# Performance work log

Measured on AMD Instinct MI355X. Metric: run time of the kernel, lower is better.

Reference implementation:

```python
import jax, jax.numpy as jnp
import numpy as np

N_NODES = 100000


def setup_inputs() -> dict:
    key = jax.random.key(0)
    k1, k2, k3, k4, k5, k6 = jax.random.split(key, 6)
    x = jax.random.normal(k1, (N_NODES, 256), dtype=jnp.float32)
    edge_index = jax.random.randint(k2, (2, 3200000), 0, N_NODES, dtype=jnp.int64)
    # GCNConv(256, 3): glorot weight + zero bias (PyG default)
    lim1 = float(np.sqrt(6.0 / (256 + 3)))
    W1 = jax.random.uniform(k3, (256, 3), minval=-lim1, maxval=lim1, dtype=jnp.float32)
    b1 = jnp.zeros((3,), dtype=jnp.float32)
    # Linear(3, 7): torch default kaiming-uniform-ish bounds
    lim2 = float(1.0 / np.sqrt(3))
    W2 = jax.random.uniform(k4, (3, 7), minval=-lim2, maxval=lim2, dtype=jnp.float32)
    b2 = jax.random.uniform(k5, (7,), minval=-lim2, maxval=lim2, dtype=jnp.float32)
    return {"x": x, "edge_index": edge_index, "W1": W1, "b1": b1, "W2": W2, "b2": b2}


def gcn_conv(x, edge_index, W, b, num_nodes):
    # PyG GCNConv: add self-loops, symmetric deg^-1/2 (A+I) deg^-1/2 normalization,
    # aggregate transformed features, then add bias.
    loop = jnp.arange(num_nodes, dtype=edge_index.dtype)
    src = jnp.concatenate([edge_index[0], loop])
    dst = jnp.concatenate([edge_index[1], loop])
    ones = jnp.ones_like(dst, dtype=x.dtype)
    deg = jax.ops.segment_sum(ones, dst, num_segments=num_nodes)  # [N]
    dinv = jnp.where(deg > 0, jax.lax.rsqrt(deg), 0.0)
    norm = dinv[src] * dinv[dst]  # [E+N]
    h = x @ W  # [N, 3] — transform BEFORE gather (small width)
    msg = h[src] * norm[:, None]  # [E+N, 3]
    agg = jax.ops.segment_sum(msg, dst, num_segments=num_nodes)  # [N, 3]
    return agg + b


def reference(x, edge_index, W1, b1, W2, b2):
    h = jax.nn.relu(gcn_conv(x, edge_index, W1, b1, x.shape[0]))  # [N, 3]
    z = h @ W2 + b2  # [N, 7]
    return (h, z)
```

## Files before the change

kernel.cpp:

```cpp
#include <hip/hip_runtime.h>
#include <stdint.h>


#define BSHIFT 8
#define BNODES 256
#define OVFCAP 32768

__device__ __forceinline__ bool ei_is64(const unsigned* __restrict__ ei) {
    const int t = threadIdx.x;
    const int nz = (t < 256) && (ei[2 * t + 1] != 0u);
    return __syncthreads_or(nz) == 0;
}

__global__ __launch_bounds__(512) void k_pre(const float* __restrict__ x,
                                             const float* __restrict__ W1,
                                             float* __restrict__ g4,
                                             const unsigned* __restrict__ ei,
                                             unsigned* __restrict__ gcount,
                                             unsigned* __restrict__ records,
                                             unsigned* __restrict__ ovf,
                                             int E, int B, int CAP, int CH,
                                             int nbin, int N) {
    const bool is64 = ei_is64(ei);
    if ((int)blockIdx.x < nbin) {
        __shared__ unsigned cnt[512], base[512], cursor[512];
        const int e0 = blockIdx.x * CH;
        const int e1 = min(E, e0 + CH);
        for (int i = threadIdx.x; i < B; i += 512) { cnt[i] = 0u; cursor[i] = 0u; }
        __syncthreads();
        const unsigned long long* e64 = (const unsigned long long*)ei;
        for (int e = e0 + threadIdx.x; e < e1; e += 512) {
            const unsigned d = is64 ? (unsigned)e64[(size_t)E + e] : ei[(size_t)E + e];
            atomicAdd(&cnt[d >> BSHIFT], 1u);
        }
        __syncthreads();
        for (int i = threadIdx.x; i < B; i += 512)
            base[i] = cnt[i] ? atomicAdd(&gcount[i], cnt[i]) : 0u;
        __syncthreads();
        unsigned* ovf_cnt = gcount + B;
        for (int e = e0 + threadIdx.x; e < e1; e += 512) {
            unsigned s, d;
            if (is64) { s = (unsigned)e64[e]; d = (unsigned)e64[(size_t)E + e]; }
            else      { s = ei[e];            d = ei[(size_t)E + e]; }
            const unsigned bb  = d >> BSHIFT;
            const unsigned idx = base[bb] + atomicAdd(&cursor[bb], 1u);
            if (idx < (unsigned)CAP) {
                records[(size_t)bb * CAP + idx] = (s << BSHIFT) | (d & (BNODES - 1));
            } else {
                const unsigned o = atomicAdd(ovf_cnt, 1u);
                if (o < (unsigned)OVFCAP) { ovf[2 * o] = s; ovf[2 * o + 1] = d; }
            }
        }
    } else {
        const int bx      = blockIdx.x - nbin;
        const int gtid    = bx * 512 + threadIdx.x;
        const int nthread = ((int)gridDim.x - nbin) * 512;
        const int lane    = threadIdx.x & 63;
        float w[4][3];
#pragma unroll
        for (int k = 0; k < 4; ++k)
#pragma unroll
            for (int c = 0; c < 3; ++c)
                w[k][c] = W1[(lane * 4 + k) * 3 + c];
        const int wave   = gtid >> 6;
        const int nwaves = nthread >> 6;
        for (int node = wave; node < N; node += nwaves) {
            const float4 v = *reinterpret_cast<const float4*>(x + (size_t)node * 256 + lane * 4);
            float s0 = v.x * w[0][0] + v.y * w[1][0] + v.z * w[2][0] + v.w * w[3][0];
            float s1 = v.x * w[0][1] + v.y * w[1][1] + v.z * w[2][1] + v.w * w[3][1];
            float s2 = v.x * w[0][2] + v.y * w[1][2] + v.z * w[2][2] + v.w * w[3][2];
#pragma unroll
            for (int off = 32; off > 0; off >>= 1) {
                s0 += __shfl_xor(s0, off, 64);
                s1 += __shfl_xor(s1, off, 64);
                s2 += __shfl_xor(s2, off, 64);
            }
            if (lane == 0)
                reinterpret_cast<float4*>(g4)[node] = make_float4(s0, s1, s2, 0.f);
        }
    }
}

__global__ __launch_bounds__(256) void k_cnt2(const unsigned* __restrict__ gcount,
                                              const unsigned* __restrict__ records,
                                              const unsigned* __restrict__ ovf,
                                              unsigned* __restrict__ pcount,
                                              int B, int CAP, int SPLIT) {
    __shared__ unsigned cnt[BNODES];
    const int b  = blockIdx.x / SPLIT;
    const int sl = blockIdx.x - b * SPLIT;
    cnt[threadIdx.x] = 0u;
    __syncthreads();
    unsigned n = gcount[b]; if (n > (unsigned)CAP) n = CAP;
    const unsigned chunk = (n + SPLIT - 1) / SPLIT;
    const unsigned lo = sl * chunk;
    const unsigned hi = (lo + chunk < n) ? lo + chunk : n;
    const unsigned* rec = records + (size_t)b * CAP;
    for (unsigned i = lo + threadIdx.x; i < hi; i += 256)
        atomicAdd(&cnt[rec[i] & (BNODES - 1)], 1u);
    if (sl == 0) {
        unsigned no = gcount[B]; if (no > (unsigned)OVFCAP) no = OVFCAP;
        for (unsigned i = threadIdx.x; i < no; i += 256) {
            const unsigned d = ovf[2 * i + 1];
            if ((int)(d >> BSHIFT) == b) atomicAdd(&cnt[d & (BNODES - 1)], 1u);
        }
    }
    __syncthreads();
    pcount[((size_t)blockIdx.x << BSHIFT) + threadIdx.x] = cnt[threadIdx.x];
}

__global__ __launch_bounds__(256) void k_dinv2(const unsigned* __restrict__ pcount,
                                               float* __restrict__ g4, int N, int SPLIT) {
    const int i = blockIdx.x * 256 + threadIdx.x;
    if (i >= N) return;
    const int b = i >> BSHIFT, t = i & (BNODES - 1);
    unsigned deg = 1u;
    for (int s = 0; s < SPLIT; ++s)
        deg += pcount[(((size_t)b * SPLIT + s) << BSHIFT) + t];
    const float r = rsqrtf((float)deg);
    const float4 h = reinterpret_cast<const float4*>(g4)[i];
    reinterpret_cast<float4*>(g4)[i] = make_float4(h.x * r, h.y * r, h.z * r, r);
}

__global__ __launch_bounds__(256) void k_msg2(const unsigned* __restrict__ gcount,
                                              const unsigned* __restrict__ records,
                                              const unsigned* __restrict__ ovf,
                                              const float* __restrict__ g4,
                                              float* __restrict__ psum,
                                              int B, int CAP, int SPLIT) {
    __shared__ float acc[BNODES * 3];
    const int b  = blockIdx.x / SPLIT;
    const int sl = blockIdx.x - b * SPLIT;
    for (int i = threadIdx.x; i < BNODES * 3; i += 256) acc[i] = 0.f;
    __syncthreads();
    unsigned n = gcount[b]; if (n > (unsigned)CAP) n = CAP;
    const unsigned chunk = (n + SPLIT - 1) / SPLIT;
    const unsigned lo = sl * chunk;
    const unsigned hi = (lo + chunk < n) ? lo + chunk : n;
    const unsigned* rec = records + (size_t)b * CAP;
    const float4* g4v = reinterpret_cast<const float4*>(g4);
    unsigned i = lo + threadIdx.x;
    for (; i + 256 < hi; i += 512) {
        const unsigned r0 = rec[i], r1 = rec[i + 256];
        const float4 ga = g4v[r0 >> BSHIFT];
        const float4 gb = g4v[r1 >> BSHIFT];
        const unsigned l0 = (r0 & (BNODES - 1)) * 3, l1 = (r1 & (BNODES - 1)) * 3;
        atomicAdd(&acc[l0 + 0], ga.x); atomicAdd(&acc[l0 + 1], ga.y); atomicAdd(&acc[l0 + 2], ga.z);
        atomicAdd(&acc[l1 + 0], gb.x); atomicAdd(&acc[l1 + 1], gb.y); atomicAdd(&acc[l1 + 2], gb.z);
    }
    if (i < hi) {
        const unsigned r0 = rec[i];
        const float4 ga = g4v[r0 >> BSHIFT];
        const unsigned l0 = (r0 & (BNODES - 1)) * 3;
        atomicAdd(&acc[l0 + 0], ga.x); atomicAdd(&acc[l0 + 1], ga.y); atomicAdd(&acc[l0 + 2], ga.z);
    }
    if (sl == 0) {
        unsigned no = gcount[B]; if (no > (unsigned)OVFCAP) no = OVFCAP;
        for (unsigned k = threadIdx.x; k < no; k += 256) {
            const unsigned d = ovf[2 * k + 1];
            if ((int)(d >> BSHIFT) == b) {
                const float4 g = g4v[ovf[2 * k]];
                const unsigned l = (d & (BNODES - 1)) * 3;
                atomicAdd(&acc[l + 0], g.x); atomicAdd(&acc[l + 1], g.y); atomicAdd(&acc[l + 2], g.z);
            }
        }
    }
    __syncthreads();
    const size_t base = ((size_t)blockIdx.x * 3) << BSHIFT;
    psum[base +   0 + threadIdx.x] = acc[threadIdx.x * 3 + 0];
    psum[base + 256 + threadIdx.x] = acc[threadIdx.x * 3 + 1];
    psum[base + 512 + threadIdx.x] = acc[threadIdx.x * 3 + 2];
}

__global__ __launch_bounds__(256) void k_fin(const float* __restrict__ psum,
                                             const float* __restrict__ g4,
                                             const float* __restrict__ b1,
                                             const float* __restrict__ W2,
                                             const float* __restrict__ b2,
                                             float* __restrict__ out, int N, int SPLIT) {
    const int i = blockIdx.x * 256 + threadIdx.x;
    if (i >= N) return;
    const int b = i >> BSHIFT, t = i & (BNODES - 1);
    float a0 = 0.f, a1 = 0.f, a2 = 0.f;
    for (int s = 0; s < SPLIT; ++s) {
        const size_t base = (((size_t)b * SPLIT + s) * 3) << BSHIFT;
        a0 += psum[base + t];
        a1 += psum[base + 256 + t];
        a2 += psum[base + 512 + t];
    }
    const float4 g = reinterpret_cast<const float4*>(g4)[i];
    const float  r = g.w;
    const float h0 = fmaxf(r * (a0 + g.x) + b1[0], 0.f);
    const float h1 = fmaxf(r * (a1 + g.y) + b1[1], 0.f);
    const float h2 = fmaxf(r * (a2 + g.z) + b1[2], 0.f);
    out[3 * (size_t)i + 0] = h0;
    out[3 * (size_t)i + 1] = h1;
    out[3 * (size_t)i + 2] = h2;
    float* z = out + (size_t)3 * N;
#pragma unroll
    for (int c = 0; c < 7; ++c)
        z[7 * (size_t)i + c] = h0 * W2[c] + h1 * W2[7 + c] + h2 * W2[14 + c] + b2[c];
}

__global__ __launch_bounds__(256) void k_xw1_fb(const float* __restrict__ x,
                                                const float* __restrict__ W1,
                                                float* __restrict__ g4,
                                                unsigned* __restrict__ zptr,
                                                int nzero, int N) {
    const int gtid = blockIdx.x * 256 + threadIdx.x;
    const int nthread = gridDim.x * 256;
    for (int i = gtid; i < nzero; i += nthread) zptr[i] = 0u;
    const int lane = threadIdx.x & 63;
    float w[4][3];
#pragma unroll
    for (int k = 0; k < 4; ++k)
#pragma unroll
        for (int c = 0; c < 3; ++c) w[k][c] = W1[(lane * 4 + k) * 3 + c];
    const int wave = gtid >> 6, nwaves = nthread >> 6;
    for (int node = wave; node < N; node += nwaves) {
        const float4 v = *reinterpret_cast<const float4*>(x + (size_t)node * 256 + lane * 4);
        float s0 = v.x * w[0][0] + v.y * w[1][0] + v.z * w[2][0] + v.w * w[3][0];
        float s1 = v.x * w[0][1] + v.y * w[1][1] + v.z * w[2][1] + v.w * w[3][1];
        float s2 = v.x * w[0][2] + v.y * w[1][2] + v.z * w[2][2] + v.w * w[3][2];
#pragma unroll
        for (int off = 32; off > 0; off >>= 1) {
            s0 += __shfl_xor(s0, off, 64);
            s1 += __shfl_xor(s1, off, 64);
            s2 += __shfl_xor(s2, off, 64);
        }
        if (lane == 0)
            reinterpret_cast<float4*>(g4)[node] = make_float4(s0, s1, s2, 0.f);
    }
}
__global__ __launch_bounds__(256) void k_deg_fb(const unsigned* __restrict__ ei,
                                                float* __restrict__ deg, int E) {
    const bool is64 = ei_is64(ei);
    const int e = blockIdx.x * 256 + threadIdx.x;
    if (e >= E) return;
    const unsigned d = is64 ? (unsigned)((const unsigned long long*)ei)[(size_t)E + e]
                            : ei[(size_t)E + e];
    atomicAdd(&deg[d], 1.0f);
}
__global__ __launch_bounds__(256) void k_dinv_fb(const float* __restrict__ deg,
                                                 float* __restrict__ g4, int N) {
    const int i = blockIdx.x * 256 + threadIdx.x;
    if (i >= N) return;
    const float r = rsqrtf(1.0f + deg[i]);
    const float4 h = reinterpret_cast<const float4*>(g4)[i];
    reinterpret_cast<float4*>(g4)[i] = make_float4(h.x * r, h.y * r, h.z * r, r);
}
__global__ __launch_bounds__(256) void k_edge_fb(const unsigned* __restrict__ ei,
                                                 const float* __restrict__ g4,
                                                 float* __restrict__ u4, int E) {
    const bool is64 = ei_is64(ei);
    const int e = blockIdx.x * 256 + threadIdx.x;
    if (e >= E) return;
    unsigned s, d;
    if (is64) {
        const unsigned long long* q = (const unsigned long long*)ei;
        s = (unsigned)q[e]; d = (unsigned)q[(size_t)E + e];
    } else {
        s = ei[e]; d = ei[(size_t)E + e];
    }
    const float4 g = reinterpret_cast<const float4*>(g4)[s];
    atomicAdd(&u4[4 * (size_t)d + 0], g.x);
    atomicAdd(&u4[4 * (size_t)d + 1], g.y);
    atomicAdd(&u4[4 * (size_t)d + 2], g.z);
}
__global__ __launch_bounds__(256) void k_final_fb(const float* __restrict__ u4,
                                                  const float* __restrict__ g4,
                                                  const float* __restrict__ b1,
                                                  const float* __restrict__ W2,
                                                  const float* __restrict__ b2,
                                                  float* __restrict__ out, int N) {
    const int i = blockIdx.x * 256 + threadIdx.x;
    if (i >= N) return;
    const float4 g = reinterpret_cast<const float4*>(g4)[i];
    const float4 u = reinterpret_cast<const float4*>(u4)[i];
    const float  r = g.w;
    const float h0 = fmaxf(r * (u.x + g.x) + b1[0], 0.f);
    const float h1 = fmaxf(r * (u.y + g.y) + b1[1], 0.f);
    const float h2 = fmaxf(r * (u.z + g.z) + b1[2], 0.f);
    out[3 * (size_t)i + 0] = h0;
    out[3 * (size_t)i + 1] = h1;
    out[3 * (size_t)i + 2] = h2;
    float* z = out + (size_t)3 * N;
#pragma unroll
    for (int c = 0; c < 7; ++c)
        z[7 * (size_t)i + c] = h0 * W2[c] + h1 * W2[7 + c] + h2 * W2[14 + c] + b2[c];
}

extern "C" void kernel_launch(void* const* d_in, const int* in_sizes, int n_in,
                              void* d_out, int out_size, void* d_ws, size_t ws_size,
                              hipStream_t stream) {
    const float*    x   = (const float*)d_in[0];
    const unsigned* ei  = (const unsigned*)d_in[1];
    const float*    W1  = (const float*)d_in[2];
    const float*    b1  = (const float*)d_in[3];
    const float*    W2  = (const float*)d_in[4];
    const float*    b2  = (const float*)d_in[5];
    float*          out = (float*)d_out;

    const int N = in_sizes[0] / 256;
    const int E = in_sizes[1] / 2;
    const int B = (N + BNODES - 1) >> BSHIFT;

    char*     ws     = (char*)d_ws;
    unsigned* gcount = (unsigned*)ws;
    size_t off = (4ull * (B + 1) + 255) & ~(size_t)255;
    float*    g4  = (float*)(ws + off);
    off = (off + 16ull * N + 255) & ~(size_t)255;
    unsigned* ovf = (unsigned*)(ws + off);
    off = (off + 8ull * OVFCAP + 255) & ~(size_t)255;
    const size_t puoff = off;

    int SPLIT = 0, CAP = 0;
    size_t rec_off = 0;
    const int sps[4] = {8, 4, 2, 1};
    for (int si = 0; si < 4; ++si) {
        const int sp = sps[si];
        const size_t ro = (puoff + 4ull * B * sp * 768 + 255) & ~(size_t)255;
        if (ws_size < ro + 4096) continue;
        long cap = (long)((ws_size - ro) / (4ull * B));
        if (cap > 12288) cap = 12288;
        if (cap >= 8960) { SPLIT = sp; CAP = (int)cap; rec_off = ro; break; }
    }

    if (SPLIT) {
        unsigned* pcount  = (unsigned*)(ws + puoff);
        float*    psum    = (float*)(ws + puoff);
        unsigned* records = (unsigned*)(ws + rec_off);
        hipMemsetAsync(gcount, 0, 4ull * (B + 1), stream);
        const int CH   = 16384;
        const int nbin = (E + CH - 1) / CH;
        const int NBX  = 2048;
        k_pre<<<nbin + NBX, 512, 0, stream>>>(x, W1, g4, ei, gcount, records, ovf,
                                              E, B, CAP, CH, nbin, N);
        k_cnt2<<<B * SPLIT, 256, 0, stream>>>(gcount, records, ovf, pcount, B, CAP, SPLIT);
        k_dinv2<<<(N + 255) / 256, 256, 0, stream>>>(pcount, g4, N, SPLIT);
        k_msg2<<<B * SPLIT, 256, 0, stream>>>(gcount, records, ovf, g4, psum, B, CAP, SPLIT);
        k_fin<<<(N + 255) / 256, 256, 0, stream>>>(psum, g4, b1, W2, b2, out, N, SPLIT);
    } else {
        float* deg = (float*)(ws + puoff);
        float* u4  = deg + N;
        k_xw1_fb<<<4096, 256, 0, stream>>>(x, W1, g4, (unsigned*)deg, 5 * N, N);
        k_deg_fb<<<(E + 255) / 256, 256, 0, stream>>>(ei, deg, E);
        k_dinv_fb<<<(N + 255) / 256, 256, 0, stream>>>(deg, g4, N);
        k_edge_fb<<<(E + 255) / 256, 256, 0, stream>>>(ei, g4, u4, E);
        k_final_fb<<<(N + 255) / 256, 256, 0, stream>>>(u4, g4, b1, W2, b2, out, N);
    }
}
```

Measured before the change: 118.4 us.

## Replace global-atomic bucket binning with fixed per-block slots in a single pass

The edge binning in k_pre no longer does a count pass followed by a global atomicAdd per bucket to reserve ranges. Each of about 190 edge chunks now writes straight into a fixed 64-slot region per destination bucket, and records its per-bucket fill count in a pcnt table. Edges are read once, using vectorized uint4 or ulonglong2 loads. The count and message kernels scan the full fixed-capacity bucket layout and skip empty slots using the pcnt counts. This removes the second pass over the edge list and the global atomics, at the cost of scanning padded slots. Any bucket that exceeds its 64 slots goes to a smaller overflow list, which is scanned serially.

```diff
diff --git a/kernel.cpp b/kernel.cpp
--- a/kernel.cpp
+++ b/kernel.cpp
@@ -4,7 +4,9 @@
 
 #define BSHIFT 8
 #define BNODES 256
-#define OVFCAP 32768
+#define OVFCAP 8192
+#define STRIDE 64
+#define PSTRIDE 192
 
 __device__ __forceinline__ bool ei_is64(const unsigned* __restrict__ ei) {
     const int t = threadIdx.x;
@@ -16,41 +18,63 @@
                                              const float* __restrict__ W1,
                                              float* __restrict__ g4,
                                              const unsigned* __restrict__ ei,
-                                             unsigned* __restrict__ gcount,
                                              unsigned* __restrict__ records,
+                                             unsigned* __restrict__ pcnt,
+                                             unsigned* __restrict__ ovf_cnt,
                                              unsigned* __restrict__ ovf,
                                              int E, int B, int CAP, int CH,
                                              int nbin, int N) {
     const bool is64 = ei_is64(ei);
     if ((int)blockIdx.x < nbin) {
-        __shared__ unsigned cnt[512], base[512], cursor[512];
+        __shared__ unsigned cursor[512];
+        for (int i = threadIdx.x; i < B; i += 512) cursor[i] = 0u;
+        __syncthreads();
         const int e0 = blockIdx.x * CH;
         const int e1 = min(E, e0 + CH);
-        for (int i = threadIdx.x; i < B; i += 512) { cnt[i] = 0u; cursor[i] = 0u; }
-        __syncthreads();
-        const unsigned long long* e64 = (const unsigned long long*)ei;
-        for (int e = e0 + threadIdx.x; e < e1; e += 512) {
-            const unsigned d = is64 ? (unsigned)e64[(size_t)E + e] : ei[(size_t)E + e];
-            atomicAdd(&cnt[d >> BSHIFT], 1u);
+        const unsigned sbase = blockIdx.x * STRIDE;
+
+        auto emit = [&](unsigned s, unsigned d) {
+            const unsigned bb  = d >> BSHIFT;
+            const unsigned idx = atomicAdd(&cursor[bb], 1u);
+            if (idx < STRIDE) {
+                records[(size_t)bb * CAP + sbase + idx] = (s << BSHIFT) | (d & (BNODES - 1));
+            } else {
+                const unsigned o = atomicAdd(ovf_cnt, 1u);
+                if (o < OVFCAP) { ovf[2 * o] = s; ovf[2 * o + 1] = d; }
+            }
+        };
+
+        const int nq = (e1 - e0) >> 2;
+        if (is64) {
+            const unsigned long long* e64 = (const unsigned long long*)ei;
+            const ulonglong2* sp = (const ulonglong2*)(e64 + e0);
+            const ulonglong2* dp = (const ulonglong2*)(e64 + (size_t)E + e0);
+            for (int q = threadIdx.x; q < nq; q += 512) {
+                const ulonglong2 sa = sp[2 * q], sb = sp[2 * q + 1];
+                const ulonglong2 da = dp[2 * q], db = dp[2 * q + 1];
+                emit((unsigned)sa.x, (unsigned)da.x);
+                emit((unsigned)sa.y, (unsigned)da.y);
+                emit((unsigned)sb.x, (unsigned)db.x);
+                emit((unsigned)sb.y, (unsigned)db.y);
+            }
+            for (int e = e0 + 4 * nq + threadIdx.x; e < e1; e += 512)
+                emit((unsigned)e64[e], (unsigned)e64[(size_t)E + e]);
+        } else {
+            const uint4* sp = (const uint4*)(ei + e0);
+            const uint4* dp = (const uint4*)(ei + (size_t)E + e0);
+            for (int q = threadIdx.x; q < nq; q += 512) {
+                const uint4 s4 = sp[q], d4 = dp[q];
+                emit(s4.x, d4.x);
+                emit(s4.y, d4.y);
+                emit(s4.z, d4.z);
+                emit(s4.w, d4.w);
+            }
+            for (int e = e0 + 4 * nq + threadIdx.x; e < e1; e += 512)
+                emit(ei[e], ei[(size_t)E + e]);
         }
         __syncthreads();
         for (int i = threadIdx.x; i < B; i += 512)
-            base[i] = cnt[i] ? atomicAdd(&gcount[i], cnt[i]) : 0u;
-        __syncthreads();
-        unsigned* ovf_cnt = gcount + B;
-        for (int e = e0 + threadIdx.x; e < e1; e += 512) {
-            unsigned s, d;
-            if (is64) { s = (unsigned)e64[e]; d = (unsigned)e64[(size_t)E + e]; }
-            else      { s = ei[e];            d = ei[(size_t)E + e]; }
-            const unsigned bb  = d >> BSHIFT;
-            const unsigned idx = base[bb] + atomicAdd(&cursor[bb], 1u);
-            if (idx < (unsigned)CAP) {
-                records[(size_t)bb * CAP + idx] = (s << BSHIFT) | (d & (BNODES - 1));
-            } else {
-                const unsigned o = atomicAdd(ovf_cnt, 1u);
-                if (o < (unsigned)OVFCAP) { ovf[2 * o] = s; ovf[2 * o + 1] = d; }
-            }
-        }
+            pcnt[(size_t)i * PSTRIDE + blockIdx.x] = min(cursor[i], (unsigned)STRIDE);
     } else {
         const int bx      = blockIdx.x - nbin;
         const int gtid    = bx * 512 + threadIdx.x;
@@ -81,25 +105,28 @@
     }
 }
 
-__global__ __launch_bounds__(256) void k_cnt2(const unsigned* __restrict__ gcount,
-                                              const unsigned* __restrict__ records,
+__global__ __launch_bounds__(256) void k_cnt2(const unsigned* __restrict__ records,
+                                              const unsigned* __restrict__ pcnt,
+                                              const unsigned* __restrict__ ovf_cnt,
                                               const unsigned* __restrict__ ovf,
                                               unsigned* __restrict__ pcount,
-                                              int B, int CAP, int SPLIT) {
+                                              int B, int CAP, int SPLIT, int nbin) {
     __shared__ unsigned cnt[BNODES];
+    __shared__ unsigned scnt[PSTRIDE];
     const int b  = blockIdx.x / SPLIT;
     const int sl = blockIdx.x - b * SPLIT;
     cnt[threadIdx.x] = 0u;
+    for (int i = threadIdx.x; i < nbin; i += 256) scnt[i] = pcnt[(size_t)b * PSTRIDE + i];
     __syncthreads();
-    unsigned n = gcount[b]; if (n > (unsigned)CAP) n = CAP;
-    const unsigned chunk = (n + SPLIT - 1) / SPLIT;
-    const unsigned lo = sl * chunk;
-    const unsigned hi = (lo + chunk < n) ? lo + chunk : n;
+    const int per = CAP / SPLIT;
+    const int lo = sl * per, hi = lo + per;
     const unsigned* rec = records + (size_t)b * CAP;
-    for (unsigned i = lo + threadIdx.x; i < hi; i += 256)
-        atomicAdd(&cnt[rec[i] & (BNODES - 1)], 1u);
+    for (int k = lo + threadIdx.x; k < hi; k += 256) {
+        if ((unsigned)(k & (STRIDE - 1)) < scnt[k >> 6])
+            atomicAdd(&cnt[rec[k] & (BNODES - 1)], 1u);
+    }
     if (sl == 0) {
-        unsigned no = gcount[B]; if (no > (unsigned)OVFCAP) no = OVFCAP;
+        unsigned no = *ovf_cnt; if (no > OVFCAP) no = OVFCAP;
         for (unsigned i = threadIdx.x; i < no; i += 256) {
             const unsigned d = ovf[2 * i + 1];
             if ((int)(d >> BSHIFT) == b) atomicAdd(&cnt[d & (BNODES - 1)], 1u);
@@ -122,46 +149,44 @@
     reinterpret_cast<float4*>(g4)[i] = make_float4(h.x * r, h.y * r, h.z * r, r);
 }
 
-__global__ __launch_bounds__(256) void k_msg2(const unsigned* __restrict__ gcount,
-                                              const unsigned* __restrict__ records,
+__global__ __launch_bounds__(256) void k_msg2(const unsigned* __restrict__ records,
+                                              const unsigned* __restrict__ pcnt,
+                                              const unsigned* __restrict__ ovf_cnt,
                                               const unsigned* __restrict__ ovf,
                                               const float* __restrict__ g4,
                                               float* __restrict__ psum,
-                                              int B, int CAP, int SPLIT) {
+                                              int B, int CAP, int SPLIT, int nbin) {
     __shared__ float acc[BNODES * 3];
+    __shared__ unsigned scnt[PSTRIDE];
     const int b  = blockIdx.x / SPLIT;
     const int sl = blockIdx.x - b * SPLIT;
     for (int i = threadIdx.x; i < BNODES * 3; i += 256) acc[i] = 0.f;
+    for (int i = threadIdx.x; i < nbin; i += 256) scnt[i] = pcnt[(size_t)b * PSTRIDE + i];
     __syncthreads();
-    unsigned n = gcount[b]; if (n > (unsigned)CAP) n = CAP;
-    const unsigned chunk = (n + SPLIT - 1) / SPLIT;
-    const unsigned lo = sl * chunk;
-    const unsigned hi = (lo + chunk < n) ? lo + chunk : n;
+    const int per = CAP / SPLIT;
+    const int lo = sl * per, hi = lo + per;
     const unsigned* rec = records + (size_t)b * CAP;
     const float4* g4v = reinterpret_cast<const float4*>(g4);
-    unsigned i = lo + threadIdx.x;
-    for (; i + 256 < hi; i += 512) {
-        const unsigned r0 = rec[i], r1 = rec[i + 256];
-        const float4 ga = g4v[r0 >> BSHIFT];
-        const float4 gb = g4v[r1 >> BSHIFT];
-        const unsigned l0 = (r0 & (BNODES - 1)) * 3, l1 = (r1 & (BNODES - 1)) * 3;
-        atomicAdd(&acc[l0 + 0], ga.x); atomicAdd(&acc[l0 + 1], ga.y); atomicAdd(&acc[l0 + 2], ga.z);
-        atomicAdd(&acc[l1 + 0], gb.x); atomicAdd(&acc[l1 + 1], gb.y); atomicAdd(&acc[l1 + 2], gb.z);
-    }
-    if (i < hi) {
-        const unsigned r0 = rec[i];
-        const float4 ga = g4v[r0 >> BSHIFT];
-        const unsigned l0 = (r0 & (BNODES - 1)) * 3;
-        atomicAdd(&acc[l0 + 0], ga.x); atomicAdd(&acc[l0 + 1], ga.y); atomicAdd(&acc[l0 + 2], ga.z);
+    for (int k = lo + threadIdx.x; k < hi; k += 256) {
+        if ((unsigned)(k & (STRIDE - 1)) < scnt[k >> 6]) {
+            const unsigned r = rec[k];
+            const float4 g = g4v[r >> BSHIFT];
+            const unsigned l = (r & (BNODES - 1)) * 3;
+            atomicAdd(&acc[l + 0], g.x);
+            atomicAdd(&acc[l + 1], g.y);
+            atomicAdd(&acc[l + 2], g.z);
+        }
     }
     if (sl == 0) {
-        unsigned no = gcount[B]; if (no > (unsigned)OVFCAP) no = OVFCAP;
-        for (unsigned k = threadIdx.x; k < no; k += 256) {
-            const unsigned d = ovf[2 * k + 1];
+        unsigned no = *ovf_cnt; if (no > OVFCAP) no = OVFCAP;
+        for (unsigned i = threadIdx.x; i < no; i += 256) {
+            const unsigned d = ovf[2 * i + 1];
             if ((int)(d >> BSHIFT) == b) {
-                const float4 g = g4v[ovf[2 * k]];
+                const float4 g = g4v[ovf[2 * i]];
                 const unsigned l = (d & (BNODES - 1)) * 3;
-                atomicAdd(&acc[l + 0], g.x); atomicAdd(&acc[l + 1], g.y); atomicAdd(&acc[l + 2], g.z);
+                atomicAdd(&acc[l + 0], g.x);
+                atomicAdd(&acc[l + 1], g.y);
+                atomicAdd(&acc[l + 2], g.z);
             }
         }
     }
@@ -305,40 +330,43 @@
     const int E = in_sizes[1] / 2;
     const int B = (N + BNODES - 1) >> BSHIFT;
 
-    char*     ws     = (char*)d_ws;
-    unsigned* gcount = (unsigned*)ws;
-    size_t off = (4ull * (B + 1) + 255) & ~(size_t)255;
+    int CH   = ((E + 189) / 190 + 3) & ~3;
+    int nbin = (E + CH - 1) / CH;
+    int CAP  = nbin * STRIDE;
+
+    char*     ws      = (char*)d_ws;
+    unsigned* ovf_cnt = (unsigned*)ws;
+    size_t off = 256;
     float*    g4  = (float*)(ws + off);
     off = (off + 16ull * N + 255) & ~(size_t)255;
     unsigned* ovf = (unsigned*)(ws + off);
     off = (off + 8ull * OVFCAP + 255) & ~(size_t)255;
+    unsigned* pcnt = (unsigned*)(ws + off);
+    off = (off + 4ull * B * PSTRIDE + 255) & ~(size_t)255;
     const size_t puoff = off;
 
-    int SPLIT = 0, CAP = 0;
+    int SPLIT = 0;
     size_t rec_off = 0;
     const int sps[4] = {8, 4, 2, 1};
     for (int si = 0; si < 4; ++si) {
         const int sp = sps[si];
         const size_t ro = (puoff + 4ull * B * sp * 768 + 255) & ~(size_t)255;
-        if (ws_size < ro + 4096) continue;
-        long cap = (long)((ws_size - ro) / (4ull * B));
-        if (cap > 12288) cap = 12288;
-        if (cap >= 8960) { SPLIT = sp; CAP = (int)cap; rec_off = ro; break; }
+        if (ws_size >= ro + 4ull * B * CAP + 4096) { SPLIT = sp; rec_off = ro; break; }
     }
 
     if (SPLIT) {
         unsigned* pcount  = (unsigned*)(ws + puoff);
         float*    psum    = (float*)(ws + puoff);
         unsigned* records = (unsigned*)(ws + rec_off);
-        hipMemsetAsync(gcount, 0, 4ull * (B + 1), stream);
-        const int CH   = 16384;
-        const int nbin = (E + CH - 1) / CH;
-        const int NBX  = 2048;
-        k_pre<<<nbin + NBX, 512, 0, stream>>>(x, W1, g4, ei, gcount, records, ovf,
-                                              E, B, CAP, CH, nbin, N);
-        k_cnt2<<<B * SPLIT, 256, 0, stream>>>(gcount, records, ovf, pcount, B, CAP, SPLIT);
+        hipMemsetAsync(ovf_cnt, 0, 4, stream);
+        const int NBX = 2048;
+        k_pre<<<nbin + NBX, 512, 0, stream>>>(x, W1, g4, ei, records, pcnt,
+                                              ovf_cnt, ovf, E, B, CAP, CH, nbin, N);
+        k_cnt2<<<B * SPLIT, 256, 0, stream>>>(records, pcnt, ovf_cnt, ovf, pcount,
+                                              B, CAP, SPLIT, nbin);
         k_dinv2<<<(N + 255) / 256, 256, 0, stream>>>(pcount, g4, N, SPLIT);
-        k_msg2<<<B * SPLIT, 256, 0, stream>>>(gcount, records, ovf, g4, psum, B, CAP, SPLIT);
+        k_msg2<<<B * SPLIT, 256, 0, stream>>>(records, pcnt, ovf_cnt, ovf, g4, psum,
+                                              B, CAP, SPLIT, nbin);
         k_fin<<<(N + 255) / 256, 256, 0, stream>>>(psum, g4, b1, W2, b2, out, N, SPLIT);
     } else {
         float* deg = (float*)(ws + puoff);
```

Result: no change. 116.5 us (-1.6%).
